# Kernel optimization log

Hardware: AMD Instinct MI355X
Metric: run time of the kernel (lower is better)

## Reference

```python
import jax, jax.numpy as jnp
import numpy as np

B, CIN, COUT = 4, 512, 64
T, H, W = 16, 32, 32


def conv1x1(x, w, b=None):
    # 1x1x1 Conv3d == per-voxel linear: w (out, in), x (b, in, t, h, w)
    y = jnp.einsum('oc,bcthw->bothw', w, x)
    if b is not None:
        y = y + b[None, :, None, None, None]
    return y


def setup_inputs() -> dict:
    key = jax.random.key(0)
    ks = jax.random.split(key, 9)
    def kaiming(k, fan_out_shape):
        out_c, in_c = fan_out_shape
        std = np.sqrt(2.0 / out_c)  # fan_out mode for 1x1x1 kernel
        return jax.random.normal(k, fan_out_shape, dtype=jnp.float32) * std
    c4, c8 = CIN // 4, CIN // 8
    return {
        'x': jax.random.normal(ks[0], (B, CIN, T, H, W), dtype=jnp.float32),
        'w_add1': kaiming(ks[1], (CIN, CIN)), 'b_add1': jnp.zeros((CIN,), jnp.float32),
        'w_add2': kaiming(ks[2], (CIN, CIN)), 'b_add2': jnp.zeros((CIN,), jnp.float32),
        'w_occ1': kaiming(ks[3], (c4, CIN)), 'b_occ1': jnp.zeros((c4,), jnp.float32),
        'w_occ2': kaiming(ks[4], (c8, c4)), 'b_occ2': jnp.zeros((c8,), jnp.float32),
        'w_occ3': kaiming(ks[5], (COUT, c8)),  # bias=False
    }


def reference(x, w_add1, b_add1, w_add2, b_add2, w_occ1, b_occ1, w_occ2, b_occ2, w_occ3):
    # feature_map = add_on_layer(x): conv -> relu -> conv
    feat = conv1x1(jax.nn.relu(conv1x1(x, w_add1, b_add1)), w_add2, b_add2)
    # occ_map = abs(occ(x)): conv -> relu -> conv -> relu -> conv(no bias)
    h = jax.nn.relu(conv1x1(x, w_occ1, b_occ1))
    h = jax.nn.relu(conv1x1(h, w_occ2, b_occ2))
    occ = jnp.abs(conv1x1(h, w_occ3))  # (B, COUT, T, H, W)
    # output with pool='avg': mean over spatial of occ[:, :, None] * feat[:, None]
    # == einsum contraction over T*H*W, avoiding the (B,COUT,CIN,T,H,W) intermediate
    S = T * H * W
    out = jnp.einsum('bothw,bcthw->boc', occ, feat) / S  # (B, COUT, CIN)
    return out
```

## Files before the change

### kernel.cpp

```cpp
#include <hip/hip_runtime.h>


#define S_TOT 16384

typedef __attribute__((ext_vector_type(8))) short bf8_t;
typedef __attribute__((ext_vector_type(4))) short s4_t;
typedef __attribute__((ext_vector_type(4))) float f4_t;

#define MFMA __builtin_amdgcn_mfma_f32_16x16x32_bf16

#define BAR_FENCE() do { __builtin_amdgcn_s_barrier(); \
                         asm volatile("" ::: "memory"); } while (0)
#define WAIT_VM8()  asm volatile("s_waitcnt vmcnt(8)" ::: "memory")
#define WAIT_VM0()  asm volatile("s_waitcnt vmcnt(0)" ::: "memory")
#define WAIT_LGKM0() asm volatile("s_waitcnt lgkmcnt(0)" ::: "memory")

__device__ __forceinline__ short f2bf(float f) {
  union { float f; unsigned u; } v; v.f = f;
  unsigned u = v.u + 0x7FFFu + ((v.u >> 16) & 1u);
  return (short)(u >> 16);
}

__device__ __forceinline__ void glds16(const void* g, void* l) {
  __builtin_amdgcn_global_load_lds(
      (const __attribute__((address_space(1))) void*)g,
      (__attribute__((address_space(3))) void*)l, 16, 0, 0);
}

__device__ __forceinline__ void stage16k(const short* g, short* lds,
                                         int wv, int lane) {
#pragma unroll
  for (int i = 0; i < 4; ++i) {
    const int off = (wv * 4 + i) * 512;
    glds16(g + off + lane * 8, lds + off);
  }
}

__global__ __launch_bounds__(256) void k_transpose(
    const float* __restrict__ x, short* __restrict__ xTs,
    const float* __restrict__ w1, const float* __restrict__ wo1,
    const float* __restrict__ wo2, const float* __restrict__ wo3,
    short* __restrict__ wb) {
  __shared__ float tls[64][129];
  const int sb = blockIdx.x, cb = blockIdx.y, b = blockIdx.z;
  const int t = threadIdx.x;
  if (cb == 0 && b == 0) {
    for (int i = sb * 256 + t; i < 339968; i += 32768) {
      if (i < 262144) {
        const int j = i >> 9, k = i & 511;
        const int di = ((j >> 7) * 8 + (k >> 6)) * 8192 +
                       ((k >> 3) & 7) * 1024 + (j & 127) * 8 + (k & 7);
        wb[di] = f2bf(w1[i]);
      } else if (i < 327680) {
        const int e = i - 262144;
        const int c4 = e >> 9, k = e & 511;
        const int di = 262144 + (k >> 6) * 8192 + ((k >> 3) & 7) * 1024 +
                       c4 * 8 + (k & 7);
        wb[di] = f2bf(wo1[e]);
      } else if (i < 335872) {
        wb[i] = f2bf(wo2[i - 327680]);
      } else {
        wb[i] = f2bf(wo3[i - 335872]);
      }
    }
  }
  {
    const int cr = t >> 2, ss = (t & 3) * 32;
    const float* src = x + ((size_t)b * 512 + cb * 64 + cr) * S_TOT +
                       sb * 128 + ss;
#pragma unroll
    for (int k = 0; k < 8; ++k) {
      f4_t v = *(const f4_t*)(src + k * 4);
#pragma unroll
      for (int j = 0; j < 4; ++j) tls[cr][ss + k * 4 + j] = v[j];
    }
  }
  __syncthreads();
  {
#pragma unroll
    for (int h = 0; h < 2; ++h) {
      const int id = h * 256 + t;
      const int s_in = id >> 2, cs = (id & 3) * 16, k8 = cs >> 3;
      alignas(16) short tmp[16];
#pragma unroll
      for (int j = 0; j < 16; ++j) tmp[j] = f2bf(tls[cs + j][s_in]);
      short* base = xTs + (((size_t)(b * 128 + sb) * 8 + cb) * 8 + k8) * 1024 +
                    s_in * 8;
      *(bf8_t*)base          = *(const bf8_t*)&tmp[0];
      *(bf8_t*)(base + 1024) = *(const bf8_t*)&tmp[8];
    }
  }
}

__global__ __launch_bounds__(256) void k_occ(
    const short* __restrict__ xTs, const short* __restrict__ wo1,
    const short* __restrict__ wo2, const short* __restrict__ wo3,
    const float* __restrict__ bo1, const float* __restrict__ bo2,
    short* __restrict__ occP, float* __restrict__ sumocc) {
  __shared__ short smem[32768];
  short* const buf0 = smem;
  short* const buf1 = smem + 16384;
  short* const h1s = buf0;
  short* const h2s = buf1;
  const int tile = blockIdx.x, b = blockIdx.y;
  const int t = threadIdx.x, lane = t & 63, wv = t >> 6;
  const int q = lane >> 4, li = lane & 15;
  const int mh = (wv & 1) * 64, nh = (wv >> 1) * 64;
  const short* xTb = xTs + (size_t)(b * 128 + tile) * 65536;
  const f4_t fz = {0.f, 0.f, 0.f, 0.f};

  f4_t hcc[4][4];
#pragma unroll
  for (int i = 0; i < 4; ++i)
#pragma unroll
    for (int j = 0; j < 4; ++j) hcc[i][j] = fz;

  stage16k(xTb, buf1, wv, lane);
  stage16k(wo1, buf1 + 8192, wv, lane);
  for (int i = 0; i < 8; ++i) {
    BAR_FENCE();
    if (i < 7) {
      short* nb_ = (i & 1) ? buf1 : buf0;
      stage16k(xTb + (i + 1) * 8192, nb_, wv, lane);
      stage16k(wo1 + (i + 1) * 8192, nb_ + 8192, wv, lane);
      WAIT_VM8();
    } else {
      WAIT_VM0();
    }
    BAR_FENCE();
    const short* xs = (i & 1) ? buf0 : buf1;
    const short* wsp = xs + 8192;
#pragma unroll
    for (int kk = 0; kk < 2; ++kk) {
      const int pl = (4 * kk + q) * 128;
      bf8_t a[4], bb[4];
#pragma unroll
      for (int ma = 0; ma < 4; ++ma)
        a[ma] = *(const bf8_t*)&wsp[(pl + mh + 16 * ma + li) * 8];
#pragma unroll
      for (int nb = 0; nb < 4; ++nb)
        bb[nb] = *(const bf8_t*)&xs[(pl + nh + 16 * nb + li) * 8];
#pragma unroll
      for (int ma = 0; ma < 4; ++ma)
#pragma unroll
        for (int nb = 0; nb < 4; ++nb)
          hcc[ma][nb] = MFMA(a[ma], bb[nb], hcc[ma][nb], 0, 0, 0);
    }
  }
  WAIT_LGKM0();
  BAR_FENCE();
#pragma unroll
  for (int ma = 0; ma < 4; ++ma) {
    const int c40 = mh + 16 * ma + 4 * q;
    f4_t bv = *(const f4_t*)(bo1 + c40);
#pragma unroll
    for (int nb = 0; nb < 4; ++nb) {
      const int sl = nh + 16 * nb + li;
      s4_t p;
#pragma unroll
      for (int r = 0; r < 4; ++r) p[r] = f2bf(fmaxf(hcc[ma][nb][r] + bv[r], 0.0f));
      *(s4_t*)&h1s[((c40 >> 3) * 128 + sl) * 8 + (c40 & 7)] = p;
    }
  }
  __syncthreads();
  f4_t a2[4][2];
#pragma unroll
  for (int i = 0; i < 4; ++i) { a2[i][0] = fz; a2[i][1] = fz; }
#pragma unroll
  for (int kk = 0; kk < 4; ++kk) {
    const int pl = (4 * kk + q) * 128;
    bf8_t a[4], bb[2];
#pragma unroll
    for (int ma = 0; ma < 4; ++ma)
      a[ma] = *(const bf8_t*)(wo2 + (size_t)(16 * ma + li) * 128 + kk * 32 + q * 8);
#pragma unroll
    for (int nb = 0; nb < 2; ++nb)
      bb[nb] = *(const bf8_t*)&h1s[(pl + 32 * wv + 16 * nb + li) * 8];
#pragma unroll
    for (int ma = 0; ma < 4; ++ma)
#pragma unroll
      for (int nb = 0; nb < 2; ++nb)
        a2[ma][nb] = MFMA(a[ma], bb[nb], a2[ma][nb], 0, 0, 0);
  }
#pragma unroll
  for (int ma = 0; ma < 4; ++ma) {
    const int c80 = 16 * ma + 4 * q;
    f4_t bv = *(const f4_t*)(bo2 + c80);
#pragma unroll
    for (int nb = 0; nb < 2; ++nb) {
      const int sl = 32 * wv + 16 * nb + li;
      s4_t p;
#pragma unroll
      for (int r = 0; r < 4; ++r) p[r] = f2bf(fmaxf(a2[ma][nb][r] + bv[r], 0.0f));
      *(s4_t*)&h2s[((c80 >> 3) * 128 + sl) * 8 + (c80 & 7)] = p;
    }
  }
  f4_t a3[4][2];
#pragma unroll
  for (int i = 0; i < 4; ++i) { a3[i][0] = fz; a3[i][1] = fz; }
#pragma unroll
  for (int kk = 0; kk < 2; ++kk) {
    const int pl = (4 * kk + q) * 128;
    bf8_t a[4], bb[2];
#pragma unroll
    for (int ma = 0; ma < 4; ++ma)
      a[ma] = *(const bf8_t*)(wo3 + (size_t)(16 * ma + li) * 64 + kk * 32 + q * 8);
#pragma unroll
    for (int nb = 0; nb < 2; ++nb)
      bb[nb] = *(const bf8_t*)&h2s[(pl + 32 * wv + 16 * nb + li) * 8];
#pragma unroll
    for (int ma = 0; ma < 4; ++ma)
#pragma unroll
      for (int nb = 0; nb < 2; ++nb)
        a3[ma][nb] = MFMA(a[ma], bb[nb], a3[ma][nb], 0, 0, 0);
  }
  short* ot = occP + (size_t)(b * 128 + tile) * 8192;
#pragma unroll
  for (int ma = 0; ma < 4; ++ma)
#pragma unroll
    for (int nb = 0; nb < 2; ++nb) {
      const int o = 16 * ma + 4 * q;
      const int sl = 32 * wv + 16 * nb + li;
#pragma unroll
      for (int r = 0; r < 4; ++r)
        ot[(sl >> 3) * 512 + (o + r) * 8 + (sl & 7)] = f2bf(fabsf(a3[ma][nb][r]));
    }
#pragma unroll
  for (int ma = 0; ma < 4; ++ma)
#pragma unroll
    for (int r = 0; r < 4; ++r) {
      float v = fabsf(a3[ma][0][r]) + fabsf(a3[ma][1][r]);
#pragma unroll
      for (int m = 1; m < 16; m <<= 1) v += __shfl_xor(v, m, 64);
      if (li == 0) atomicAdd(&sumocc[b * 64 + 16 * ma + 4 * q + r], v);
    }
}

__global__ __launch_bounds__(256) void k_feat(
    const short* __restrict__ xTs, const short* __restrict__ w1s,
    const float* __restrict__ b1, const short* __restrict__ occP,
    float* __restrict__ M) {
  __shared__ short smem[32768];
  short* const buf0 = smem;
  short* const buf1 = smem + 16384;
  short* const r1s = buf0;
  const int sg = blockIdx.x, cb = blockIdx.y, b = blockIdx.z;
  const int t = threadIdx.x, lane = t & 63, wv = t >> 6;
  const int q = lane >> 4, li = lane & 15;
  const int mh = (wv & 1) * 64, nh = (wv >> 1) * 64;
  const short* w1b = w1s + (size_t)cb * 65536;
  const f4_t fz = {0.f, 0.f, 0.f, 0.f};

  float biasv[4];
#pragma unroll
  for (int nb = 0; nb < 4; ++nb) biasv[nb] = b1[cb * 128 + nh + 16 * nb + li];

  f4_t macc[4][2];
#pragma unroll
  for (int i = 0; i < 4; ++i) { macc[i][0] = fz; macc[i][1] = fz; }

  {
    const short* xT0 = xTs + (size_t)(b * 128 + sg * 4) * 65536;
    stage16k(xT0, buf1, wv, lane);
    stage16k(w1b, buf1 + 8192, wv, lane);
  }

  for (int tt = 0; tt < 4; ++tt) {
    const int st = sg * 4 + tt;
    const short* xTb = xTs + (size_t)(b * 128 + st) * 65536;
    f4_t acc[4][4];
#pragma unroll
    for (int i = 0; i < 4; ++i)
#pragma unroll
      for (int j = 0; j < 4; ++j) acc[i][j] = fz;

    for (int i = 0; i < 8; ++i) {
      BAR_FENCE();
      if (i < 7) {
        short* nb_ = (i & 1) ? buf1 : buf0;
        stage16k(xTb + (i + 1) * 8192, nb_, wv, lane);
        stage16k(w1b + (i + 1) * 8192, nb_ + 8192, wv, lane);
        WAIT_VM8();
      } else {
        WAIT_VM0();
      }
      BAR_FENCE();
      const short* xs = (i & 1) ? buf0 : buf1;
      const short* wsp = xs + 8192;
#pragma unroll
      for (int kk = 0; kk < 2; ++kk) {
        const int pl = (4 * kk + q) * 128;
        bf8_t a[4], bb[4];
#pragma unroll
        for (int ma = 0; ma < 4; ++ma)
          a[ma] = *(const bf8_t*)&xs[(pl + mh + 16 * ma + li) * 8];
#pragma unroll
        for (int nb = 0; nb < 4; ++nb)
          bb[nb] = *(const bf8_t*)&wsp[(pl + nh + 16 * nb + li) * 8];
#pragma unroll
        for (int ma = 0; ma < 4; ++ma)
#pragma unroll
          for (int nb = 0; nb < 4; ++nb)
            acc[ma][nb] = MFMA(a[ma], bb[nb], acc[ma][nb], 0, 0, 0);
      }
    }
    WAIT_LGKM0();
    BAR_FENCE();
#pragma unroll
    for (int ma = 0; ma < 4; ++ma) {
      const int sl0 = mh + 16 * ma + 4 * q;
#pragma unroll
      for (int nb = 0; nb < 4; ++nb) {
        const int jl = nh + 16 * nb + li;
        s4_t p;
#pragma unroll
        for (int r = 0; r < 4; ++r)
          p[r] = f2bf(fmaxf(acc[ma][nb][r] + biasv[nb], 0.0f));
        *(s4_t*)&r1s[((sl0 >> 3) * 128 + jl) * 8 + (sl0 & 7)] = p;
      }
    }
    WAIT_LGKM0();
    BAR_FENCE();
    const short* ot = occP + (size_t)(b * 128 + st) * 8192;
    bf8_t af[4][4];
#pragma unroll
    for (int kc = 0; kc < 4; ++kc)
#pragma unroll
      for (int ma = 0; ma < 4; ++ma)
        af[ma][kc] = *(const bf8_t*)(ot + ((kc * 4 + q) * 64 + 16 * ma + li) * 8);
    if (tt < 3) {
      stage16k(xTb + 65536, buf1, wv, lane);
      stage16k(w1b, buf1 + 8192, wv, lane);
    }
#pragma unroll
    for (int kc = 0; kc < 4; ++kc) {
      const int pl = (4 * kc + q) * 128;
      bf8_t bb[2];
#pragma unroll
      for (int nb = 0; nb < 2; ++nb)
        bb[nb] = *(const bf8_t*)&r1s[(pl + 32 * wv + 16 * nb + li) * 8];
#pragma unroll
      for (int ma = 0; ma < 4; ++ma)
#pragma unroll
        for (int nb = 0; nb < 2; ++nb)
          macc[ma][nb] = MFMA(af[ma][kc], bb[nb], macc[ma][nb], 0, 0, 0);
    }
  }
#pragma unroll
  for (int ma = 0; ma < 4; ++ma)
#pragma unroll
    for (int nb = 0; nb < 2; ++nb) {
      const int jg = cb * 128 + 32 * wv + 16 * nb + li;
#pragma unroll
      for (int r = 0; r < 4; ++r) {
        const int o = 16 * ma + 4 * q + r;
        atomicAdd(&M[((size_t)b * 64 + o) * 512 + jg], macc[ma][nb][r]);
      }
    }
}

__global__ __launch_bounds__(256) void k_out(
    const float* __restrict__ M, const float* __restrict__ sumocc,
    const float* __restrict__ w2, const float* __restrict__ b2,
    float* __restrict__ out) {
  __shared__ float Mlds[16][516];
  __shared__ float Wlds[16][516];
  const int cg = blockIdx.x, og = blockIdx.y, b = blockIdx.z;
  const int t = threadIdx.x;
  const float* Msrc = M + ((size_t)b * 64 + og * 16) * 512;
  const float* Wsrc = w2 + (size_t)cg * 16 * 512;
#pragma unroll
  for (int k = 0; k < 8; ++k) {
    const int fi = k * 256 + t;
    const int row = fi >> 7, col = (fi & 127) * 4;
    *(f4_t*)&Mlds[row][col] = *(const f4_t*)(Msrc + row * 512 + col);
    *(f4_t*)&Wlds[row][col] = *(const f4_t*)(Wsrc + row * 512 + col);
  }
  __syncthreads();
  const int o = t >> 4, c = t & 15;
  float s0 = 0.f, s1 = 0.f;
#pragma unroll 8
  for (int j = 0; j < 512; j += 8) {
    f4_t m0 = *(const f4_t*)&Mlds[o][j];
    f4_t w0 = *(const f4_t*)&Wlds[c][j];
    f4_t m1 = *(const f4_t*)&Mlds[o][j + 4];
    f4_t w1 = *(const f4_t*)&Wlds[c][j + 4];
    s0 += m0[0] * w0[0] + m0[1] * w0[1] + m0[2] * w0[2] + m0[3] * w0[3];
    s1 += m1[0] * w1[0] + m1[1] * w1[1] + m1[2] * w1[2] + m1[3] * w1[3];
  }
  const int og_ = og * 16 + o, cg_ = cg * 16 + c;
  out[((size_t)b * 64 + og_) * 512 + cg_] =
      ((s0 + s1) + sumocc[b * 64 + og_] * b2[cg_]) * (1.0f / 16384.0f);
}

extern "C" void kernel_launch(void* const* d_in, const int* in_sizes, int n_in,
                              void* d_out, int out_size, void* d_ws, size_t ws_size,
                              hipStream_t stream) {
  (void)in_sizes; (void)n_in; (void)out_size; (void)ws_size;
  const float* x      = (const float*)d_in[0];
  const float* w_add1 = (const float*)d_in[1];
  const float* b_add1 = (const float*)d_in[2];
  const float* w_add2 = (const float*)d_in[3];
  const float* b_add2 = (const float*)d_in[4];
  const float* w_occ1 = (const float*)d_in[5];
  const float* b_occ1 = (const float*)d_in[6];
  const float* w_occ2 = (const float*)d_in[7];
  const float* b_occ2 = (const float*)d_in[8];
  const float* w_occ3 = (const float*)d_in[9];

  char* ws = (char*)d_ws;
  short* xTs     = (short*)(ws);
  short* wb      = (short*)(ws + 67108864);
  short* occP    = (short*)(ws + 67788800);
  float* M       = (float*)(ws + 76177408);
  float* sumocc  = (float*)(ws + 76701696);

  hipMemsetAsync(M, 0, 524288 + 1024, stream);
  k_transpose<<<dim3(128, 8, 4), dim3(256), 0, stream>>>(
      x, xTs, w_add1, w_occ1, w_occ2, w_occ3, wb);

  const short* w1sp = wb;
  const short* wbo1 = wb + 262144;
  const short* wbo2 = wb + 327680;
  const short* wbo3 = wb + 335872;
  k_occ<<<dim3(128, 4), dim3(256), 0, stream>>>(xTs, wbo1, wbo2, wbo3,
                                                b_occ1, b_occ2, occP, sumocc);
  k_feat<<<dim3(32, 4, 4), dim3(256), 0, stream>>>(xTs, w1sp, b_add1, occP, M);
  k_out<<<dim3(32, 4, 4), dim3(256), 0, stream>>>(M, sumocc, w_add2, b_add2,
                                                  (float*)d_out);
}
```

Before: 375.9 us.

## Use 8 waves per block in occ and feat kernels, spread weight conversion

Doubles the block size of the occupancy and feature GEMM kernels from 4 to 8 waves. Each wave now computes half the output tile, and the LDS staging per wave is halved with a matching vmcnt wait. The weight bf16 conversion in the transpose kernel is also spread over all blocks, one element per thread, instead of looping inside a single slice of blocks. This aims for more latency hiding per CU and less register pressure per wave, at the cost of more barrier participants and less per-wave reuse of A fragments.

```diff
diff --git a/kernel.cpp b/kernel.cpp
--- a/kernel.cpp
+++ b/kernel.cpp
@@ -11,7 +11,7 @@
 
 #define BAR_FENCE() do { __builtin_amdgcn_s_barrier(); \
                          asm volatile("" ::: "memory"); } while (0)
-#define WAIT_VM8()  asm volatile("s_waitcnt vmcnt(8)" ::: "memory")
+#define WAIT_VM4()  asm volatile("s_waitcnt vmcnt(4)" ::: "memory")
 #define WAIT_VM0()  asm volatile("s_waitcnt vmcnt(0)" ::: "memory")
 #define WAIT_LGKM0() asm volatile("s_waitcnt lgkmcnt(0)" ::: "memory")
 
@@ -27,11 +27,11 @@
       (__attribute__((address_space(3))) void*)l, 16, 0, 0);
 }
 
-__device__ __forceinline__ void stage16k(const short* g, short* lds,
-                                         int wv, int lane) {
-#pragma unroll
-  for (int i = 0; i < 4; ++i) {
-    const int off = (wv * 4 + i) * 512;
+__device__ __forceinline__ void stage16k8(const short* g, short* lds,
+                                          int wv, int lane) {
+#pragma unroll
+  for (int i = 0; i < 2; ++i) {
+    const int off = (wv * 2 + i) * 512;
     glds16(g + off + lane * 8, lds + off);
   }
 }
@@ -44,8 +44,10 @@
   __shared__ float tls[64][129];
   const int sb = blockIdx.x, cb = blockIdx.y, b = blockIdx.z;
   const int t = threadIdx.x;
-  if (cb == 0 && b == 0) {
-    for (int i = sb * 256 + t; i < 339968; i += 32768) {
+  {
+    const int bid = (b * 8 + cb) * 128 + sb;
+    const int i = bid * 256 + t;
+    if (i < 339968) {
       if (i < 262144) {
         const int j = i >> 9, k = i & 511;
         const int di = ((j >> 7) * 8 + (k >> 6)) * 8192 +
@@ -92,7 +94,7 @@
   }
 }
 
-__global__ __launch_bounds__(256) void k_occ(
+__global__ __launch_bounds__(512) void k_occ(
     const short* __restrict__ xTs, const short* __restrict__ wo1,
     const short* __restrict__ wo2, const short* __restrict__ wo3,
     const float* __restrict__ bo1, const float* __restrict__ bo2,
@@ -105,25 +107,25 @@
   const int tile = blockIdx.x, b = blockIdx.y;
   const int t = threadIdx.x, lane = t & 63, wv = t >> 6;
   const int q = lane >> 4, li = lane & 15;
-  const int mh = (wv & 1) * 64, nh = (wv >> 1) * 64;
+  const int mh1 = (wv & 1) * 64;
+  const int nhs = (wv >> 1) * 32;
+  const int swc = wv * 16;
   const short* xTb = xTs + (size_t)(b * 128 + tile) * 65536;
   const f4_t fz = {0.f, 0.f, 0.f, 0.f};
 
-  f4_t hcc[4][4];
-#pragma unroll
-  for (int i = 0; i < 4; ++i)
-#pragma unroll
-    for (int j = 0; j < 4; ++j) hcc[i][j] = fz;
-
-  stage16k(xTb, buf1, wv, lane);
-  stage16k(wo1, buf1 + 8192, wv, lane);
+  f4_t hcc[4][2];
+#pragma unroll
+  for (int i = 0; i < 4; ++i) { hcc[i][0] = fz; hcc[i][1] = fz; }
+
+  stage16k8(xTb, buf1, wv, lane);
+  stage16k8(wo1, buf1 + 8192, wv, lane);
   for (int i = 0; i < 8; ++i) {
     BAR_FENCE();
     if (i < 7) {
       short* nb_ = (i & 1) ? buf1 : buf0;
-      stage16k(xTb + (i + 1) * 8192, nb_, wv, lane);
-      stage16k(wo1 + (i + 1) * 8192, nb_ + 8192, wv, lane);
-      WAIT_VM8();
+      stage16k8(xTb + (i + 1) * 8192, nb_, wv, lane);
+      stage16k8(wo1 + (i + 1) * 8192, nb_ + 8192, wv, lane);
+      WAIT_VM4();
     } else {
       WAIT_VM0();
     }
@@ -133,17 +135,17 @@
 #pragma unroll
     for (int kk = 0; kk < 2; ++kk) {
       const int pl = (4 * kk + q) * 128;
-      bf8_t a[4], bb[4];
+      bf8_t a[4], bb[2];
 #pragma unroll
       for (int ma = 0; ma < 4; ++ma)
-        a[ma] = *(const bf8_t*)&wsp[(pl + mh + 16 * ma + li) * 8];
-#pragma unroll
-      for (int nb = 0; nb < 4; ++nb)
-        bb[nb] = *(const bf8_t*)&xs[(pl + nh + 16 * nb + li) * 8];
+        a[ma] = *(const bf8_t*)&wsp[(pl + mh1 + 16 * ma + li) * 8];
+#pragma unroll
+      for (int nb = 0; nb < 2; ++nb)
+        bb[nb] = *(const bf8_t*)&xs[(pl + nhs + 16 * nb + li) * 8];
 #pragma unroll
       for (int ma = 0; ma < 4; ++ma)
 #pragma unroll
-        for (int nb = 0; nb < 4; ++nb)
+        for (int nb = 0; nb < 2; ++nb)
           hcc[ma][nb] = MFMA(a[ma], bb[nb], hcc[ma][nb], 0, 0, 0);
     }
   }
@@ -151,11 +153,11 @@
   BAR_FENCE();
 #pragma unroll
   for (int ma = 0; ma < 4; ++ma) {
-    const int c40 = mh + 16 * ma + 4 * q;
+    const int c40 = mh1 + 16 * ma + 4 * q;
     f4_t bv = *(const f4_t*)(bo1 + c40);
 #pragma unroll
-    for (int nb = 0; nb < 4; ++nb) {
-      const int sl = nh + 16 * nb + li;
+    for (int nb = 0; nb < 2; ++nb) {
+      const int sl = nhs + 16 * nb + li;
       s4_t p;
 #pragma unroll
       for (int r = 0; r < 4; ++r) p[r] = f2bf(fmaxf(hcc[ma][nb][r] + bv[r], 0.0f));
@@ -163,80 +165,67 @@
     }
   }
   __syncthreads();
-  f4_t a2[4][2];
-#pragma unroll
-  for (int i = 0; i < 4; ++i) { a2[i][0] = fz; a2[i][1] = fz; }
+  f4_t a2[4];
+#pragma unroll
+  for (int i = 0; i < 4; ++i) a2[i] = fz;
 #pragma unroll
   for (int kk = 0; kk < 4; ++kk) {
     const int pl = (4 * kk + q) * 128;
-    bf8_t a[4], bb[2];
+    bf8_t a[4], bb;
 #pragma unroll
     for (int ma = 0; ma < 4; ++ma)
       a[ma] = *(const bf8_t*)(wo2 + (size_t)(16 * ma + li) * 128 + kk * 32 + q * 8);
-#pragma unroll
-    for (int nb = 0; nb < 2; ++nb)
-      bb[nb] = *(const bf8_t*)&h1s[(pl + 32 * wv + 16 * nb + li) * 8];
+    bb = *(const bf8_t*)&h1s[(pl + swc + li) * 8];
 #pragma unroll
     for (int ma = 0; ma < 4; ++ma)
-#pragma unroll
-      for (int nb = 0; nb < 2; ++nb)
-        a2[ma][nb] = MFMA(a[ma], bb[nb], a2[ma][nb], 0, 0, 0);
+      a2[ma] = MFMA(a[ma], bb, a2[ma], 0, 0, 0);
   }
 #pragma unroll
   for (int ma = 0; ma < 4; ++ma) {
     const int c80 = 16 * ma + 4 * q;
     f4_t bv = *(const f4_t*)(bo2 + c80);
-#pragma unroll
-    for (int nb = 0; nb < 2; ++nb) {
-      const int sl = 32 * wv + 16 * nb + li;
-      s4_t p;
-#pragma unroll
-      for (int r = 0; r < 4; ++r) p[r] = f2bf(fmaxf(a2[ma][nb][r] + bv[r], 0.0f));
-      *(s4_t*)&h2s[((c80 >> 3) * 128 + sl) * 8 + (c80 & 7)] = p;
-    }
-  }
-  f4_t a3[4][2];
-#pragma unroll
-  for (int i = 0; i < 4; ++i) { a3[i][0] = fz; a3[i][1] = fz; }
+    const int sl = swc + li;
+    s4_t p;
+#pragma unroll
+    for (int r = 0; r < 4; ++r) p[r] = f2bf(fmaxf(a2[ma][r] + bv[r], 0.0f));
+    *(s4_t*)&h2s[((c80 >> 3) * 128 + sl) * 8 + (c80 & 7)] = p;
+  }
+  f4_t a3[4];
+#pragma unroll
+  for (int i = 0; i < 4; ++i) a3[i] = fz;
 #pragma unroll
   for (int kk = 0; kk < 2; ++kk) {
     const int pl = (4 * kk + q) * 128;
-    bf8_t a[4], bb[2];
+    bf8_t a[4], bb;
 #pragma unroll
     for (int ma = 0; ma < 4; ++ma)
       a[ma] = *(const bf8_t*)(wo3 + (size_t)(16 * ma + li) * 64 + kk * 32 + q * 8);
-#pragma unroll
-    for (int nb = 0; nb < 2; ++nb)
-      bb[nb] = *(const bf8_t*)&h2s[(pl + 32 * wv + 16 * nb + li) * 8];
+    bb = *(const bf8_t*)&h2s[(pl + swc + li) * 8];
 #pragma unroll
     for (int ma = 0; ma < 4; ++ma)
-#pragma unroll
-      for (int nb = 0; nb < 2; ++nb)
-        a3[ma][nb] = MFMA(a[ma], bb[nb], a3[ma][nb], 0, 0, 0);
+      a3[ma] = MFMA(a[ma], bb, a3[ma], 0, 0, 0);
   }
   short* ot = occP + (size_t)(b * 128 + tile) * 8192;
 #pragma unroll
+  for (int ma = 0; ma < 4; ++ma) {
+    const int o = 16 * ma + 4 * q;
+    const int sl = swc + li;
+#pragma unroll
+    for (int r = 0; r < 4; ++r)
+      ot[(sl >> 3) * 512 + (o + r) * 8 + (sl & 7)] = f2bf(fabsf(a3[ma][r]));
+  }
+#pragma unroll
   for (int ma = 0; ma < 4; ++ma)
 #pragma unroll
-    for (int nb = 0; nb < 2; ++nb) {
-      const int o = 16 * ma + 4 * q;
-      const int sl = 32 * wv + 16 * nb + li;
-#pragma unroll
-      for (int r = 0; r < 4; ++r)
-        ot[(sl >> 3) * 512 + (o + r) * 8 + (sl & 7)] = f2bf(fabsf(a3[ma][nb][r]));
-    }
-#pragma unroll
-  for (int ma = 0; ma < 4; ++ma)
-#pragma unroll
     for (int r = 0; r < 4; ++r) {
-      float v = fabsf(a3[ma][0][r]) + fabsf(a3[ma][1][r]);
+      float v = fabsf(a3[ma][r]);
 #pragma unroll
       for (int m = 1; m < 16; m <<= 1) v += __shfl_xor(v, m, 64);
       if (li == 0) atomicAdd(&sumocc[b * 64 + 16 * ma + 4 * q + r], v);
     }
 }
 
-__global__ __launch_bounds__(256) void k_feat(
+__global__ __launch_bounds__(512) void k_feat(
     const short* __restrict__ xTs, const short* __restrict__ w1s,
     const float* __restrict__ b1, const short* __restrict__ occP,
     float* __restrict__ M) {
@@ -247,40 +236,40 @@
   const int sg = blockIdx.x, cb = blockIdx.y, b = blockIdx.z;
   const int t = threadIdx.x, lane = t & 63, wv = t >> 6;
   const int q = lane >> 4, li = lane & 15;
-  const int mh = (wv & 1) * 64, nh = (wv >> 1) * 64;
+  const int mh1 = (wv & 1) * 64;
+  const int nhs = (wv >> 1) * 32;
+  const int jwc = wv * 16;
   const short* w1b = w1s + (size_t)cb * 65536;
   const f4_t fz = {0.f, 0.f, 0.f, 0.f};
 
-  float biasv[4];
-#pragma unroll
-  for (int nb = 0; nb < 4; ++nb) biasv[nb] = b1[cb * 128 + nh + 16 * nb + li];
-
-  f4_t macc[4][2];
-#pragma unroll
-  for (int i = 0; i < 4; ++i) { macc[i][0] = fz; macc[i][1] = fz; }
+  float biasv[2];
+  biasv[0] = b1[cb * 128 + nhs + li];
+  biasv[1] = b1[cb * 128 + nhs + 16 + li];
+
+  f4_t macc[4];
+#pragma unroll
+  for (int i = 0; i < 4; ++i) macc[i] = fz;
 
   {
     const short* xT0 = xTs + (size_t)(b * 128 + sg * 4) * 65536;
-    stage16k(xT0, buf1, wv, lane);
-    stage16k(w1b, buf1 + 8192, wv, lane);
+    stage16k8(xT0, buf1, wv, lane);
+    stage16k8(w1b, buf1 + 8192, wv, lane);
   }
 
   for (int tt = 0; tt < 4; ++tt) {
     const int st = sg * 4 + tt;
     const short* xTb = xTs + (size_t)(b * 128 + st) * 65536;
-    f4_t acc[4][4];
-#pragma unroll
-    for (int i = 0; i < 4; ++i)
-#pragma unroll
-      for (int j = 0; j < 4; ++j) acc[i][j] = fz;
+    f4_t acc[4][2];
+#pragma unroll
+    for (int i = 0; i < 4; ++i) { acc[i][0] = fz; acc[i][1] = fz; }
 
     for (int i = 0; i < 8; ++i) {
       BAR_FENCE();
       if (i < 7) {
         short* nb_ = (i & 1) ? buf1 : buf0;
-        stage16k(xTb + (i + 1) * 8192, nb_, wv, lane);
-        stage16k(w1b + (i + 1) * 8192, nb_ + 8192, wv, lane);
-        WAIT_VM8();
+        stage16k8(xTb + (i + 1) * 8192, nb_, wv, lane);
+        stage16k8(w1b + (i + 1) * 8192, nb_ + 8192, wv, lane);
+        WAIT_VM4();
       } else {
         WAIT_VM0();
       }
@@ -290,17 +279,17 @@
 #pragma unroll
       for (int kk = 0; kk < 2; ++kk) {
         const int pl = (4 * kk + q) * 128;
-        bf8_t a[4], bb[4];
+        bf8_t a[4], bb[2];
 #pragma unroll
         for (int ma = 0; ma < 4; ++ma)
-          a[ma] = *(const bf8_t*)&xs[(pl + mh + 16 * ma + li) * 8];
-#pragma unroll
-        for (int nb = 0; nb < 4; ++nb)
-          bb[nb] = *(const bf8_t*)&wsp[(pl + nh + 16 * nb + li) * 8];
+          a[ma] = *(const bf8_t*)&xs[(pl + mh1 + 16 * ma + li) * 8];
+#pragma unroll
+        for (int nb = 0; nb < 2; ++nb)
+          bb[nb] = *(const bf8_t*)&wsp[(pl + nhs + 16 * nb + li) * 8];
 #pragma unroll
         for (int ma = 0; ma < 4; ++ma)
 #pragma unroll
-          for (int nb = 0; nb < 4; ++nb)
+          for (int nb = 0; nb < 2; ++nb)
             acc[ma][nb] = MFMA(a[ma], bb[nb], acc[ma][nb], 0, 0, 0);
       }
     }
@@ -308,10 +297,10 @@
     BAR_FENCE();
 #pragma unroll
     for (int ma = 0; ma < 4; ++ma) {
-      const int sl0 = mh + 16 * ma + 4 * q;
-#pragma unroll
-      for (int nb = 0; nb < 4; ++nb) {
-        const int jl = nh + 16 * nb + li;
+      const int sl0 = mh1 + 16 * ma + 4 * q;
+#pragma unroll
+      for (int nb = 0; nb < 2; ++nb) {
+        const int jl = nhs + 16 * nb + li;
         s4_t p;
 #pragma unroll
         for (int r = 0; r < 4; ++r)
@@ -327,36 +316,29 @@
     for (int kc = 0; kc < 4; ++kc)
 #pragma unroll
       for (int ma = 0; ma < 4; ++ma)
-        af[ma][kc] = *(const bf8_t*)(ot + ((kc * 4 + q) * 64 + 16 * ma + li) * 8);
+        af[kc][ma] = *(const bf8_t*)(ot + ((kc * 4 + q) * 64 + 16 * ma + li) * 8);
     if (tt < 3) {
-      stage16k(xTb + 65536, buf1, wv, lane);
-      stage16k(w1b, buf1 + 8192, wv, lane);
+      stage16k8(xTb + 65536, buf1, wv, lane);
+      stage16k8(w1b, buf1 + 8192, wv, lane);
     }
 #pragma unroll
     for (int kc = 0; kc < 4; ++kc) {
       const int pl = (4 * kc + q) * 128;
-      bf8_t bb[2];
-#pragma unroll
-      for (int nb = 0; nb < 2; ++nb)
-        bb[nb] = *(const bf8_t*)&r1s[(pl + 32 * wv + 16 * nb + li) * 8];
+      bf8_t bb = *(const bf8_t*)&r1s[(pl + jwc + li) * 8];
 #pragma unroll
       for (int ma = 0; ma < 4; ++ma)
-#pragma unroll
-        for (int nb = 0; nb < 2; ++nb)
-          macc[ma][nb] = MFMA(af[ma][kc], bb[nb], macc[ma][nb], 0, 0, 0);
-    }
-  }
-#pragma unroll
-  for (int ma = 0; ma < 4; ++ma)
-#pragma unroll
-    for (int nb = 0; nb < 2; ++nb) {
-      const int jg = cb * 128 + 32 * wv + 16 * nb + li;
-#pragma unroll
-      for (int r = 0; r < 4; ++r) {
-        const int o = 16 * ma + 4 * q + r;
-        atomicAdd(&M[((size_t)b * 64 + o) * 512 + jg], macc[ma][nb][r]);
-      }
-    }
+        macc[ma] = MFMA(af[kc][ma], bb, macc[ma], 0, 0, 0);
+    }
+  }
+#pragma unroll
+  for (int ma = 0; ma < 4; ++ma) {
+    const int jg = cb * 128 + jwc + li;
+#pragma unroll
+    for (int r = 0; r < 4; ++r) {
+      const int o = 16 * ma + 4 * q + r;
+      atomicAdd(&M[((size_t)b * 64 + o) * 512 + jg], macc[ma][r]);
+    }
+  }
 }
 
 __global__ __launch_bounds__(256) void k_out(
@@ -423,9 +405,9 @@
   const short* wbo1 = wb + 262144;
   const short* wbo2 = wb + 327680;
   const short* wbo3 = wb + 335872;
-  k_occ<<<dim3(128, 4), dim3(256), 0, stream>>>(xTs, wbo1, wbo2, wbo3,
+  k_occ<<<dim3(128, 4), dim3(512), 0, stream>>>(xTs, wbo1, wbo2, wbo3,
                                                 b_occ1, b_occ2, occP, sumocc);
-  k_feat<<<dim3(32, 4, 4), dim3(256), 0, stream>>>(xTs, w1sp, b_add1, occP, M);
+  k_feat<<<dim3(32, 4, 4), dim3(512), 0, stream>>>(xTs, w1sp, b_add1, occP, M);
   k_out<<<dim3(32, 4, 4), dim3(256), 0, stream>>>(M, sumocc, w_add2, b_add2,
                                                   (float*)d_out);
 }
```

New measurement: 434.9 us. +15.7%, slower.

## Read weight operands from global instead of staging in LDS; spread weight conversion across blocks

Applied to the files above, without the earlier changes.

The occ and feat GEMM loops no longer stage weight tiles into LDS. Each wave loads its weight fragments directly from global memory (expected to hit in cache), which halves the async LDS staging traffic and lowers the vmcnt wait threshold. The feat kernel gets its own r1s region, so one barrier pair before the epilogue is dropped, and the occ kernel's LDS footprint shrinks, which may raise occupancy. The transpose kernel now spreads weight bf16 conversion across all blocks instead of only the first slice. The cost is possible global-load latency exposed at the MFMA operands, and the vmcnt accounting now has to cover the extra direct global loads.

```diff
diff --git a/kernel.cpp b/kernel.cpp
--- a/kernel.cpp
+++ b/kernel.cpp
@@ -11,7 +11,7 @@
 
 #define BAR_FENCE() do { __builtin_amdgcn_s_barrier(); \
                          asm volatile("" ::: "memory"); } while (0)
-#define WAIT_VM8()  asm volatile("s_waitcnt vmcnt(8)" ::: "memory")
+#define WAIT_VM4()  asm volatile("s_waitcnt vmcnt(4)" ::: "memory")
 #define WAIT_VM0()  asm volatile("s_waitcnt vmcnt(0)" ::: "memory")
 #define WAIT_LGKM0() asm volatile("s_waitcnt lgkmcnt(0)" ::: "memory")
 
@@ -44,8 +44,10 @@
   __shared__ float tls[64][129];
   const int sb = blockIdx.x, cb = blockIdx.y, b = blockIdx.z;
   const int t = threadIdx.x;
-  if (cb == 0 && b == 0) {
-    for (int i = sb * 256 + t; i < 339968; i += 32768) {
+  {
+    const int bid = (b * 8 + cb) * 128 + sb;
+    const int i = bid * 256 + t;
+    if (i < 339968) {
       if (i < 262144) {
         const int j = i >> 9, k = i & 511;
         const int di = ((j >> 7) * 8 + (k >> 6)) * 8192 +
@@ -97,11 +99,11 @@
     const short* __restrict__ wo2, const short* __restrict__ wo3,
     const float* __restrict__ bo1, const float* __restrict__ bo2,
     short* __restrict__ occP, float* __restrict__ sumocc) {
-  __shared__ short smem[32768];
+  __shared__ short smem[24576];
   short* const buf0 = smem;
-  short* const buf1 = smem + 16384;
-  short* const h1s = buf0;
-  short* const h2s = buf1;
+  short* const buf1 = smem + 8192;
+  short* const h1s = smem;
+  short* const h2s = smem + 16384;
   const int tile = blockIdx.x, b = blockIdx.y;
   const int t = threadIdx.x, lane = t & 63, wv = t >> 6;
   const int q = lane >> 4, li = lane & 15;
@@ -116,27 +118,25 @@
     for (int j = 0; j < 4; ++j) hcc[i][j] = fz;
 
   stage16k(xTb, buf1, wv, lane);
-  stage16k(wo1, buf1 + 8192, wv, lane);
   for (int i = 0; i < 8; ++i) {
     BAR_FENCE();
     if (i < 7) {
       short* nb_ = (i & 1) ? buf1 : buf0;
       stage16k(xTb + (i + 1) * 8192, nb_, wv, lane);
-      stage16k(wo1 + (i + 1) * 8192, nb_ + 8192, wv, lane);
-      WAIT_VM8();
+      WAIT_VM4();
     } else {
       WAIT_VM0();
     }
     BAR_FENCE();
     const short* xs = (i & 1) ? buf0 : buf1;
-    const short* wsp = xs + 8192;
+    const short* og = wo1 + i * 8192;
 #pragma unroll
     for (int kk = 0; kk < 2; ++kk) {
       const int pl = (4 * kk + q) * 128;
       bf8_t a[4], bb[4];
 #pragma unroll
       for (int ma = 0; ma < 4; ++ma)
-        a[ma] = *(const bf8_t*)&wsp[(pl + mh + 16 * ma + li) * 8];
+        a[ma] = *(const bf8_t*)&og[(pl + mh + 16 * ma + li) * 8];
 #pragma unroll
       for (int nb = 0; nb < 4; ++nb)
         bb[nb] = *(const bf8_t*)&xs[(pl + nh + 16 * nb + li) * 8];
@@ -241,9 +241,9 @@
     const float* __restrict__ b1, const short* __restrict__ occP,
     float* __restrict__ M) {
   __shared__ short smem[32768];
-  short* const buf0 = smem;
-  short* const buf1 = smem + 16384;
-  short* const r1s = buf0;
+  short* const r1s = smem;
+  short* const buf0 = smem + 16384;
+  short* const buf1 = smem + 24576;
   const int sg = blockIdx.x, cb = blockIdx.y, b = blockIdx.z;
   const int t = threadIdx.x, lane = t & 63, wv = t >> 6;
   const int q = lane >> 4, li = lane & 15;
@@ -259,11 +259,7 @@
 #pragma unroll
   for (int i = 0; i < 4; ++i) { macc[i][0] = fz; macc[i][1] = fz; }
 
-  {
-    const short* xT0 = xTs + (size_t)(b * 128 + sg * 4) * 65536;
-    stage16k(xT0, buf1, wv, lane);
-    stage16k(w1b, buf1 + 8192, wv, lane);
-  }
+  stage16k(xTs + (size_t)(b * 128 + sg * 4) * 65536, buf1, wv, lane);
 
   for (int tt = 0; tt < 4; ++tt) {
     const int st = sg * 4 + tt;
@@ -279,14 +275,13 @@
       if (i < 7) {
         short* nb_ = (i & 1) ? buf1 : buf0;
         stage16k(xTb + (i + 1) * 8192, nb_, wv, lane);
-        stage16k(w1b + (i + 1) * 8192, nb_ + 8192, wv, lane);
-        WAIT_VM8();
+        WAIT_VM4();
       } else {
         WAIT_VM0();
       }
       BAR_FENCE();
       const short* xs = (i & 1) ? buf0 : buf1;
-      const short* wsp = xs + 8192;
+      const short* wg = w1b + i * 8192;
 #pragma unroll
       for (int kk = 0; kk < 2; ++kk) {
         const int pl = (4 * kk + q) * 128;
@@ -296,7 +291,7 @@
           a[ma] = *(const bf8_t*)&xs[(pl + mh + 16 * ma + li) * 8];
 #pragma unroll
         for (int nb = 0; nb < 4; ++nb)
-          bb[nb] = *(const bf8_t*)&wsp[(pl + nh + 16 * nb + li) * 8];
+          bb[nb] = *(const bf8_t*)&wg[(pl + nh + 16 * nb + li) * 8];
 #pragma unroll
         for (int ma = 0; ma < 4; ++ma)
 #pragma unroll
@@ -304,8 +299,6 @@
             acc[ma][nb] = MFMA(a[ma], bb[nb], acc[ma][nb], 0, 0, 0);
       }
     }
-    WAIT_LGKM0();
-    BAR_FENCE();
 #pragma unroll
     for (int ma = 0; ma < 4; ++ma) {
       const int sl0 = mh + 16 * ma + 4 * q;
@@ -327,11 +320,8 @@
     for (int kc = 0; kc < 4; ++kc)
 #pragma unroll
       for (int ma = 0; ma < 4; ++ma)
-        af[ma][kc] = *(const bf8_t*)(ot + ((kc * 4 + q) * 64 + 16 * ma + li) * 8);
-    if (tt < 3) {
-      stage16k(xTb + 65536, buf1, wv, lane);
-      stage16k(w1b, buf1 + 8192, wv, lane);
-    }
+        af[kc][ma] = *(const bf8_t*)(ot + ((kc * 4 + q) * 64 + 16 * ma + li) * 8);
+    if (tt < 3) stage16k(xTb + 65536, buf1, wv, lane);
 #pragma unroll
     for (int kc = 0; kc < 4; ++kc) {
       const int pl = (4 * kc + q) * 128;
@@ -343,7 +333,7 @@
       for (int ma = 0; ma < 4; ++ma)
 #pragma unroll
         for (int nb = 0; nb < 2; ++nb)
-          macc[ma][nb] = MFMA(af[ma][kc], bb[nb], macc[ma][nb], 0, 0, 0);
+          macc[ma][nb] = MFMA(af[kc][ma], bb[nb], macc[ma][nb], 0, 0, 0);
     }
   }
 #pragma unroll
```

Result: no change. 382.8 us (+1.8%).

## Fuse x transpose/bf16 conversion into occupancy kernel, split weight conversion out

Applied to the files above, without the earlier changes.

Merges the x transpose-and-convert pass into the occupancy-branch kernel. Each block now loads its fp32 x slab, transposes it through LDS, uses the bf16 chunk directly for the first occupancy GEMM, and also writes it to global for the feature kernel. This removes one read of the bf16 transposed x and one kernel launch. The weight conversion moves to its own small kernel. In exchange the occ kernel loses its async global-to-LDS double buffering, reads wo1 fragments straight from global memory, and adds extra barriers and LDS traffic per K-chunk. Launching only 512 blocks for the whole x read may also limit bandwidth. A register-array index swap in the feature kernel is cosmetic.

```diff
diff --git a/kernel.cpp b/kernel.cpp
--- a/kernel.cpp
+++ b/kernel.cpp
@@ -36,47 +36,72 @@
   }
 }
 
-__global__ __launch_bounds__(256) void k_transpose(
-    const float* __restrict__ x, short* __restrict__ xTs,
+__global__ __launch_bounds__(256) void k_convert(
     const float* __restrict__ w1, const float* __restrict__ wo1,
     const float* __restrict__ wo2, const float* __restrict__ wo3,
-    short* __restrict__ wb) {
-  __shared__ float tls[64][129];
-  const int sb = blockIdx.x, cb = blockIdx.y, b = blockIdx.z;
-  const int t = threadIdx.x;
-  if (cb == 0 && b == 0) {
-    for (int i = sb * 256 + t; i < 339968; i += 32768) {
-      if (i < 262144) {
-        const int j = i >> 9, k = i & 511;
-        const int di = ((j >> 7) * 8 + (k >> 6)) * 8192 +
-                       ((k >> 3) & 7) * 1024 + (j & 127) * 8 + (k & 7);
-        wb[di] = f2bf(w1[i]);
-      } else if (i < 327680) {
-        const int e = i - 262144;
-        const int c4 = e >> 9, k = e & 511;
-        const int di = 262144 + (k >> 6) * 8192 + ((k >> 3) & 7) * 1024 +
-                       c4 * 8 + (k & 7);
-        wb[di] = f2bf(wo1[e]);
-      } else if (i < 335872) {
-        wb[i] = f2bf(wo2[i - 327680]);
-      } else {
-        wb[i] = f2bf(wo3[i - 335872]);
-      }
-    }
-  }
-  {
-    const int cr = t >> 2, ss = (t & 3) * 32;
-    const float* src = x + ((size_t)b * 512 + cb * 64 + cr) * S_TOT +
-                       sb * 128 + ss;
+    short* __restrict__ dst) {
+  int i = blockIdx.x * 256 + threadIdx.x;
+  if (i < 262144) {
+    const int j = i >> 9, k = i & 511;
+    const int di = ((j >> 7) * 8 + (k >> 6)) * 8192 + ((k >> 3) & 7) * 1024 +
+                   (j & 127) * 8 + (k & 7);
+    dst[di] = f2bf(w1[i]);
+  } else if (i < 327680) {
+    const int e = i - 262144;
+    const int c4 = e >> 9, k = e & 511;
+    const int di = 262144 + (k >> 6) * 8192 + ((k >> 3) & 7) * 1024 +
+                   c4 * 8 + (k & 7);
+    dst[di] = f2bf(wo1[e]);
+  } else if (i < 335872) {
+    dst[i] = f2bf(wo2[i - 327680]);
+  } else if (i < 339968) {
+    dst[i] = f2bf(wo3[i - 335872]);
+  }
+}
+
+__global__ __launch_bounds__(256) void k_toc(
+    const float* __restrict__ x, short* __restrict__ xTs,
+    const short* __restrict__ wo1, const short* __restrict__ wo2,
+    const short* __restrict__ wo3, const float* __restrict__ bo1,
+    const float* __restrict__ bo2,
+    short* __restrict__ occP, float* __restrict__ sumocc) {
+  __shared__ __align__(16) char smem_raw[49408];
+  float (*tls)[129] = (float (*)[129])smem_raw;
+  short* const xchunk = (short*)(smem_raw + 33024);
+  short* const h1s = (short*)smem_raw;
+  short* const h2s = xchunk;
+  const int tile = blockIdx.x, b = blockIdx.y;
+  const int t = threadIdx.x, lane = t & 63, wv = t >> 6;
+  const int q = lane >> 4, li = lane & 15;
+  const int mh = (wv & 1) * 64, nh = (wv >> 1) * 64;
+  const f4_t fz = {0.f, 0.f, 0.f, 0.f};
+
+  const int cr = t >> 2, ss = (t & 3) * 32;
+  const float* xb = x + ((size_t)b * 512 + cr) * S_TOT + tile * 128 + ss;
+
+  f4_t hcc[4][4];
+#pragma unroll
+  for (int i = 0; i < 4; ++i)
+#pragma unroll
+    for (int j = 0; j < 4; ++j) hcc[i][j] = fz;
+
+  f4_t xr[8];
+#pragma unroll
+  for (int k = 0; k < 8; ++k) xr[k] = *(const f4_t*)(xb + k * 4);
+
+  for (int i = 0; i < 8; ++i) {
 #pragma unroll
     for (int k = 0; k < 8; ++k) {
-      f4_t v = *(const f4_t*)(src + k * 4);
+      f4_t v = xr[k];
 #pragma unroll
       for (int j = 0; j < 4; ++j) tls[cr][ss + k * 4 + j] = v[j];
     }
-  }
-  __syncthreads();
-  {
+    __syncthreads();
+    if (i < 7) {
+      const float* nsrc = xb + (size_t)(i + 1) * 64 * S_TOT;
+#pragma unroll
+      for (int k = 0; k < 8; ++k) xr[k] = *(const f4_t*)(nsrc + k * 4);
+    }
 #pragma unroll
     for (int h = 0; h < 2; ++h) {
       const int id = h * 256 + t;
@@ -84,62 +109,26 @@
       alignas(16) short tmp[16];
 #pragma unroll
       for (int j = 0; j < 16; ++j) tmp[j] = f2bf(tls[cs + j][s_in]);
-      short* base = xTs + (((size_t)(b * 128 + sb) * 8 + cb) * 8 + k8) * 1024 +
-                    s_in * 8;
-      *(bf8_t*)base          = *(const bf8_t*)&tmp[0];
-      *(bf8_t*)(base + 1024) = *(const bf8_t*)&tmp[8];
-    }
-  }
-}
-
-__global__ __launch_bounds__(256) void k_occ(
-    const short* __restrict__ xTs, const short* __restrict__ wo1,
-    const short* __restrict__ wo2, const short* __restrict__ wo3,
-    const float* __restrict__ bo1, const float* __restrict__ bo2,
-    short* __restrict__ occP, float* __restrict__ sumocc) {
-  __shared__ short smem[32768];
-  short* const buf0 = smem;
-  short* const buf1 = smem + 16384;
-  short* const h1s = buf0;
-  short* const h2s = buf1;
-  const int tile = blockIdx.x, b = blockIdx.y;
-  const int t = threadIdx.x, lane = t & 63, wv = t >> 6;
-  const int q = lane >> 4, li = lane & 15;
-  const int mh = (wv & 1) * 64, nh = (wv >> 1) * 64;
-  const short* xTb = xTs + (size_t)(b * 128 + tile) * 65536;
-  const f4_t fz = {0.f, 0.f, 0.f, 0.f};
-
-  f4_t hcc[4][4];
-#pragma unroll
-  for (int i = 0; i < 4; ++i)
-#pragma unroll
-    for (int j = 0; j < 4; ++j) hcc[i][j] = fz;
-
-  stage16k(xTb, buf1, wv, lane);
-  stage16k(wo1, buf1 + 8192, wv, lane);
-  for (int i = 0; i < 8; ++i) {
-    BAR_FENCE();
-    if (i < 7) {
-      short* nb_ = (i & 1) ? buf1 : buf0;
-      stage16k(xTb + (i + 1) * 8192, nb_, wv, lane);
-      stage16k(wo1 + (i + 1) * 8192, nb_ + 8192, wv, lane);
-      WAIT_VM8();
-    } else {
-      WAIT_VM0();
-    }
-    BAR_FENCE();
-    const short* xs = (i & 1) ? buf0 : buf1;
-    const short* wsp = xs + 8192;
+      short* lb = xchunk + k8 * 1024 + s_in * 8;
+      *(bf8_t*)lb          = *(const bf8_t*)&tmp[0];
+      *(bf8_t*)(lb + 1024) = *(const bf8_t*)&tmp[8];
+      short* gb = xTs + (((size_t)(b * 128 + tile) * 8 + i) * 8 + k8) * 1024 +
+                  s_in * 8;
+      *(bf8_t*)gb          = *(const bf8_t*)&tmp[0];
+      *(bf8_t*)(gb + 1024) = *(const bf8_t*)&tmp[8];
+    }
+    __syncthreads();
+    const short* og = wo1 + i * 8192;
 #pragma unroll
     for (int kk = 0; kk < 2; ++kk) {
       const int pl = (4 * kk + q) * 128;
       bf8_t a[4], bb[4];
 #pragma unroll
       for (int ma = 0; ma < 4; ++ma)
-        a[ma] = *(const bf8_t*)&wsp[(pl + mh + 16 * ma + li) * 8];
+        a[ma] = *(const bf8_t*)&og[(pl + mh + 16 * ma + li) * 8];
 #pragma unroll
       for (int nb = 0; nb < 4; ++nb)
-        bb[nb] = *(const bf8_t*)&xs[(pl + nh + 16 * nb + li) * 8];
+        bb[nb] = *(const bf8_t*)&xchunk[(pl + nh + 16 * nb + li) * 8];
 #pragma unroll
       for (int ma = 0; ma < 4; ++ma)
 #pragma unroll
@@ -147,8 +136,7 @@
           hcc[ma][nb] = MFMA(a[ma], bb[nb], hcc[ma][nb], 0, 0, 0);
     }
   }
-  WAIT_LGKM0();
-  BAR_FENCE();
+  __syncthreads();
 #pragma unroll
   for (int ma = 0; ma < 4; ++ma) {
     const int c40 = mh + 16 * ma + 4 * q;
@@ -327,7 +315,7 @@
     for (int kc = 0; kc < 4; ++kc)
 #pragma unroll
       for (int ma = 0; ma < 4; ++ma)
-        af[ma][kc] = *(const bf8_t*)(ot + ((kc * 4 + q) * 64 + 16 * ma + li) * 8);
+        af[kc][ma] = *(const bf8_t*)(ot + ((kc * 4 + q) * 64 + 16 * ma + li) * 8);
     if (tt < 3) {
       stage16k(xTb + 65536, buf1, wv, lane);
       stage16k(w1b, buf1 + 8192, wv, lane);
@@ -343,7 +331,7 @@
       for (int ma = 0; ma < 4; ++ma)
 #pragma unroll
         for (int nb = 0; nb < 2; ++nb)
-          macc[ma][nb] = MFMA(af[ma][kc], bb[nb], macc[ma][nb], 0, 0, 0);
+          macc[ma][nb] = MFMA(af[kc][ma], bb[nb], macc[ma][nb], 0, 0, 0);
     }
   }
 #pragma unroll
@@ -416,15 +404,14 @@
   float* sumocc  = (float*)(ws + 76701696);
 
   hipMemsetAsync(M, 0, 524288 + 1024, stream);
-  k_transpose<<<dim3(128, 8, 4), dim3(256), 0, stream>>>(
-      x, xTs, w_add1, w_occ1, w_occ2, w_occ3, wb);
+  k_convert<<<dim3(1328), dim3(256), 0, stream>>>(w_add1, w_occ1, w_occ2, w_occ3, wb);
 
   const short* w1sp = wb;
   const short* wbo1 = wb + 262144;
   const short* wbo2 = wb + 327680;
   const short* wbo3 = wb + 335872;
-  k_occ<<<dim3(128, 4), dim3(256), 0, stream>>>(xTs, wbo1, wbo2, wbo3,
-                                                b_occ1, b_occ2, occP, sumocc);
+  k_toc<<<dim3(128, 4), dim3(256), 0, stream>>>(
+      x, xTs, wbo1, wbo2, wbo3, b_occ1, b_occ2, occP, sumocc);
   k_feat<<<dim3(32, 4, 4), dim3(256), 0, stream>>>(xTs, w1sp, b_add1, occP, M);
   k_out<<<dim3(32, 4, 4), dim3(256), 0, stream>>>(M, sumocc, w_add2, b_add2,
                                                   (float*)d_out);
```

New measurement: 350.8 us. 6.7% less time.
